# Kernel tuning notes

Measured on AMD Instinct MI355X. Metric: run time of the kernel, lower is better.

## Reference

```python
import jax, jax.numpy as jnp
import numpy as np

B, N, D, H = 256, 40, 256, 256      # molecules, atoms/molecule, pc_hidden, pred_hidden
nS, nC, nB = 40, 5, 5               # n_SYMBOLS, n_FORMAL_CHARGES, n_BOND_TYPES
NEG_SLOPE = 0.01                    # F.leaky_relu default


def _lrelu(x):
    return jnp.where(x >= 0, x, NEG_SLOPE * x)


def setup_inputs() -> dict:
    key = jax.random.key(0)
    ks = jax.random.split(key, 7)
    def w(k, shape, fan_in):
        return jax.random.normal(k, shape, jnp.float32) / np.float32(np.sqrt(fan_in))
    return {
        "yhat": jax.random.normal(ks[0], (B, N, D), jnp.float32),
        "Ws1": w(ks[1], (D, H), D),      "bs1": jnp.zeros((H,), jnp.float32),
        "Ws2": w(ks[2], (H, nS), H),     "bs2": jnp.zeros((nS,), jnp.float32),
        "Wc1": w(ks[3], (D, H), D),      "bc1": jnp.zeros((H,), jnp.float32),
        "Wc2": w(ks[4], (H, nC), H),     "bc2": jnp.zeros((nC,), jnp.float32),
        "Wb1": w(ks[5], (2 * D, H), 2 * D), "bb1": jnp.zeros((H,), jnp.float32),
        "Wb2": w(ks[6], (H, nB), H),     "bb2": jnp.zeros((nB,), jnp.float32),
    }


def reference(yhat, Ws1, bs1, Ws2, bs2, Wc1, bc1, Wc2, bc2, Wb1, bb1, Wb2, bb2):
    # Per-atom symbol / charge heads (2-layer MLP with leaky_relu)
    symbols = _lrelu(yhat @ Ws1 + bs1) @ Ws2 + bs2          # [B, N, nS]
    charges = _lrelu(yhat @ Wc1 + bc1) @ Wc2 + bc2          # [B, N, nC]

    # Pairwise bond head: concat(x_i, x_j) @ Wb1 == x_i @ Wb1[:D] + x_j @ Wb1[D:]
    # (avoids materializing the [B, N, N, 2D] concat tensor)
    p1 = yhat @ Wb1[:D]                                      # [B, N, H]
    p2 = yhat @ Wb1[D:]                                      # [B, N, H]
    h = _lrelu(p1[:, :, None, :] + p2[:, None, :, :] + bb1)  # [B, N, N, H]
    bonds = h @ Wb2 + bb2                                    # [B, N, N, nB]
    bonds = bonds + jnp.swapaxes(bonds, 1, 2)                # symmetrize (i,j)+(j,i)

    return (symbols.reshape(-1, nS),
            charges.reshape(-1, nC),
            bonds.reshape(-1, nB))
```

## Files before the change

### kernel.cpp

```cpp
#include <hip/hip_runtime.h>
#include <hip/hip_bf16.h>

typedef unsigned short u16;
typedef __attribute__((ext_vector_type(4))) int   int4v;
typedef __attribute__((ext_vector_type(4))) unsigned int uint4v;
typedef __attribute__((ext_vector_type(4))) unsigned short ushort4v;
typedef __attribute__((ext_vector_type(4))) float floatx4;
typedef __attribute__((ext_vector_type(8))) short bf16x8;
typedef _Float16 half8 __attribute__((ext_vector_type(8)));
typedef _Float16 half2v __attribute__((ext_vector_type(2)));

#define LRELU_NS 0.01f
#define SK 264

__device__ __forceinline__ float bitsToF(unsigned int b) {
    union { unsigned int u; float f; } v; v.u = b << 16; return v.f;
}
__device__ __forceinline__ u16 f2bf(float f) {
    __hip_bfloat16 h = __float2bfloat16(f);
    return *reinterpret_cast<u16*>(&h);
}
__device__ __forceinline__ float lrelu(float v) {
    return fmaxf(v, LRELU_NS * v);
}
__device__ __forceinline__ u16 ldW(const void* p, int i, int isF32) {
    return isF32 ? f2bf(((const float*)p)[i]) : ((const u16*)p)[i];
}
__device__ __forceinline__ float ldF(const void* p, int i, int isF32) {
    return isF32 ? ((const float*)p)[i]
                 : bitsToF((unsigned int)((const u16*)p)[i]);
}
__device__ __forceinline__ u16 f2h_bits(float f) {
    union { _Float16 h; u16 u; } v; v.h = (_Float16)f; return v.u;
}
__device__ __forceinline__ u16 ldWh(const void* p, int i, int isF32) {
    float f = isF32 ? ((const float*)p)[i]
                    : bitsToF((unsigned int)((const u16*)p)[i]);
    return f2h_bits(f);
}
__device__ __forceinline__ half2v u2h2(unsigned int x) {
    union { unsigned int u; half2v h; } v; v.u = x; return v.h;
}
__device__ __forceinline__ unsigned int h22u(half2v x) {
    union { half2v h; unsigned int u; } v; v.h = x; return v.u;
}

__device__ __forceinline__ int computeIsF32(const u16* y, int* cnt, int t) {
    if (t == 0) *cnt = 0;
    __syncthreads();
    if (t < 256) {
        u16 v = y[2 * t];
        int e = (v >> 7) & 0xFF;
        if (v == 0 || (e >= 96 && e < 160)) atomicAdd(cnt, 1);
    }
    __syncthreads();
    return (*cnt < 192) ? 1 : 0;
}

__global__ __launch_bounds__(256) void pack_kernel(
    const void* __restrict__ yhat,
    const void* __restrict__ Ws1, const void* __restrict__ Wc1,
    const void* __restrict__ Wb1, const void* __restrict__ Ws2,
    const void* __restrict__ Wc2,
    const void* __restrict__ bs1, const void* __restrict__ bc1,
    const void* __restrict__ bb1, const void* __restrict__ bs2,
    const void* __restrict__ bc2, const void* __restrict__ bb2,
    u16* __restrict__ WallT, u16* __restrict__ W2T, float* __restrict__ biasF)
{
    __shared__ int fcnt;
    const int bid = blockIdx.x, t = threadIdx.x;
    const int isF32 = computeIsF32((const u16*)yhat, &fcnt, t);
    if (bid < 64) {
        __shared__ u16 tile[64][65];
        const int c0 = (bid & 15) * 64;
        const int k0 = (bid >> 4) * 64;
        const void* src; int coff; int roff = 0;
        if (c0 < 256)      { src = Ws1; coff = c0; }
        else if (c0 < 512) { src = Wc1; coff = c0 - 256; }
        else if (c0 < 768) { src = Wb1; coff = c0 - 512; }
        else               { src = Wb1; coff = c0 - 768; roff = 256; }
        const int cc = t & 63, kk0 = t >> 6;
        #pragma unroll
        for (int i = 0; i < 16; ++i) {
            int kk = kk0 + i * 4;
            tile[kk][cc] = ldW(src, (k0 + kk + roff) * 256 + coff + cc, isF32);
        }
        __syncthreads();
        const int kk2 = t & 63, cc0 = t >> 6;
        #pragma unroll
        for (int i = 0; i < 16; ++i) {
            int cc2 = cc0 + i * 4;
            WallT[(c0 + cc2) * 256 + (k0 + kk2)] = tile[kk2][cc2];
        }
    } else if (bid < 128) {
        int e2 = (bid - 64) * 256 + t;
        int c = e2 >> 8, k = e2 & 255;
        u16 v = 0;
        if (c < 40)                 v = ldW(Ws2, k * 40 + c, isF32);
        else if (c >= 48 && c < 53) v = ldW(Wc2, k * 5 + (c - 48), isF32);
        W2T[c * 256 + k] = v;
    } else {
        int idx = (bid - 128) * 256 + t;
        float v = 0.f;
        if (idx < 256)       v = ldF(bs1, idx, isF32);
        else if (idx < 512)  v = ldF(bc1, idx - 256, isF32);
        else if (idx < 768)  v = ldF(bb1, idx - 512, isF32);
        else if (idx < 808)  v = ldF(bs2, idx - 768, isF32);
        else if (idx < 813)  v = ldF(bc2, idx - 808, isF32);
        else if (idx >= 816 && idx < 821) v = ldF(bb2, idx - 816, isF32);
        biasF[idx] = v;
    }
}

__global__ __launch_bounds__(256) void heads_kernel(
    const void* __restrict__ Xv, const u16* __restrict__ WallT,
    const u16* __restrict__ W2T, const float* __restrict__ biasF,
    void* __restrict__ outv)
{
    __shared__ u16 Xs[64 * SK];
    __shared__ u16 Hb[64 * SK];
    __shared__ int fcnt;
    const int t = threadIdx.x;
    const int bm0 = blockIdx.x * 64;
    const int head = blockIdx.y;
    const int isF32 = computeIsF32((const u16*)Xv, &fcnt, t);

    if (isF32) {
        const floatx4* __restrict__ src = (const floatx4*)((const float*)Xv + bm0 * 256);
        #pragma unroll
        for (int it = 0; it < 16; ++it) {
            int cid = t + it * 256;
            int row = cid >> 6, ch = cid & 63;
            floatx4 f = src[cid];
            ushort4v u;
            u[0] = f2bf(f[0]); u[1] = f2bf(f[1]); u[2] = f2bf(f[2]); u[3] = f2bf(f[3]);
            *(ushort4v*)&Xs[row * SK + ch * 4] = u;
        }
    } else {
        const int4v* __restrict__ src = (const int4v*)((const u16*)Xv + bm0 * 256);
        #pragma unroll
        for (int it = 0; it < 8; ++it) {
            int cid = t + it * 256;
            int row = cid >> 5, ch = cid & 31;
            *(int4v*)&Xs[row * SK + ch * 8] = src[cid];
        }
    }
    __syncthreads();

    const int w = t >> 6, l = t & 63;
    const int ml = l & 15, kq = l >> 4, r0 = kq * 4;

    for (int n = 0; n < 4; ++n) {
        const int ct = w + 4 * n;
        floatx4 acc[4] = {};
        #pragma unroll
        for (int ks = 0; ks < 8; ++ks) {
            const int k0 = ks * 32 + kq * 8;
            bf16x8 bf = *(const bf16x8*)&WallT[(head * 256 + ct * 16 + ml) * 256 + k0];
            #pragma unroll
            for (int mt = 0; mt < 4; ++mt) {
                bf16x8 a = *(const bf16x8*)&Xs[(mt * 16 + ml) * SK + k0];
                acc[mt] = __builtin_amdgcn_mfma_f32_16x16x32_bf16(a, bf, acc[mt], 0, 0, 0);
            }
        }
        const int col = ct * 16 + ml;
        const float bias = biasF[head * 256 + col];
        #pragma unroll
        for (int mt = 0; mt < 4; ++mt)
            #pragma unroll
            for (int r = 0; r < 4; ++r)
                Hb[(mt * 16 + r0 + r) * SK + col] = f2bf(lrelu(acc[mt][r] + bias));
    }
    __syncthreads();

    const int nct = (head == 0) ? 3 : 1;
    const int c0  = (head == 0) ? 0 : 48;
    floatx4 acc2[3] = {};
    #pragma unroll
    for (int ks = 0; ks < 8; ++ks) {
        const int k0 = ks * 32 + kq * 8;
        bf16x8 a = *(const bf16x8*)&Hb[(w * 16 + ml) * SK + k0];
        #pragma unroll
        for (int j = 0; j < 3; ++j) {
            if (j < nct) {
                bf16x8 bf = *(const bf16x8*)&W2T[(c0 + j * 16 + ml) * 256 + k0];
                acc2[j] = __builtin_amdgcn_mfma_f32_16x16x32_bf16(a, bf, acc2[j], 0, 0, 0);
            }
        }
    }
    #pragma unroll
    for (int j = 0; j < 3; ++j) {
        if (j < nct) {
            const int col = j * 16 + ml;
            const int lim = (head == 0) ? 40 : 5;
            if (col < lim) {
                const float bias = biasF[(head == 0 ? 768 : 808) + col];
                #pragma unroll
                for (int r = 0; r < 4; ++r) {
                    const int row = bm0 + w * 16 + r0 + r;
                    const int o = (head == 0) ? row * 40 + col
                                              : 409600 + row * 5 + col;
                    const float v = acc2[j][r] + bias;
                    if (isF32) ((float*)outv)[o] = v;
                    else ((__hip_bfloat16*)outv)[o] = __float2bfloat16(v);
                }
            }
        }
    }
}

__global__ __launch_bounds__(512) void bonds3_kernel(
    const void* __restrict__ Xv, const u16* __restrict__ WallT,
    const void* __restrict__ Wb2, const float* __restrict__ biasF,
    void* __restrict__ outv)
{
    __shared__ u16 Xm[48 * SK];
    __shared__ u16 P1L[48 * SK];
    __shared__ u16 P2L[48 * SK];
    __shared__ u16 WsB[5 * 264];
    __shared__ int fcnt;
    const int t = threadIdx.x;
    const int b = blockIdx.x >> 1;
    const int h = blockIdx.x & 1;
    const int isF32 = computeIsF32((const u16*)Xv, &fcnt, t);

    if (isF32) {
        const floatx4* __restrict__ src = (const floatx4*)((const float*)Xv + b * 10240);
        #pragma unroll
        for (int s = 0; s < 5; ++s) {
            int cid = t + s * 512;
            int row = cid >> 6, ch = cid & 63;
            floatx4 f = src[cid];
            ushort4v u;
            u[0] = f2bf(f[0]); u[1] = f2bf(f[1]); u[2] = f2bf(f[2]); u[3] = f2bf(f[3]);
            *(ushort4v*)&Xm[row * SK + ch * 4] = u;
        }
        {
            int row = 40 + (t >> 6), ch = t & 63;
            ushort4v z = {0, 0, 0, 0};
            *(ushort4v*)&Xm[row * SK + ch * 4] = z;
        }
    } else {
        const int4v* __restrict__ src = (const int4v*)((const u16*)Xv + b * 10240);
        #pragma unroll
        for (int s = 0; s < 3; ++s) {
            int cid = t + s * 512;
            int row = cid >> 5, ch = cid & 31;
            if (cid < 1280) *(int4v*)&Xm[row * SK + ch * 8] = src[cid];
            else { int4v z = {0, 0, 0, 0}; *(int4v*)&Xm[row * SK + ch * 8] = z; }
        }
    }
    #pragma unroll
    for (int s = 0; s < 3; ++s) {
        int e2 = t + s * 512;
        if (e2 < 1280) {
            int c = e2 >> 8, k = e2 & 255;
            WsB[c * 264 + k] = ldWh(Wb2, k * 5 + c, isF32);
        }
    }
    __syncthreads();

    const int w = t >> 6, l = t & 63;
    const int ml = l & 15, kq = l >> 4, r0 = kq * 4;

    for (int n = 0; n < 4; ++n) {
        const int gc = (w + 8 * n) * 16 + ml;
        floatx4 acc[3] = {};
        #pragma unroll
        for (int ks = 0; ks < 8; ++ks) {
            const int k0 = ks * 32 + kq * 8;
            bf16x8 bf = *(const bf16x8*)&WallT[(512 + gc) * 256 + k0];
            #pragma unroll
            for (int i = 0; i < 3; ++i) {
                bf16x8 a = *(const bf16x8*)&Xm[(i * 16 + ml) * SK + k0];
                acc[i] = __builtin_amdgcn_mfma_f32_16x16x32_bf16(a, bf, acc[i], 0, 0, 0);
            }
        }
        u16* dst = (gc < 256) ? P1L : P2L;
        const int col = gc & 255;
        const float bias = (gc < 256) ? biasF[512 + gc] : 0.f;
        #pragma unroll
        for (int i = 0; i < 3; ++i)
            #pragma unroll
            for (int r = 0; r < 4; ++r)
                dst[(i * 16 + r0 + r) * SK + col] = f2h_bits(acc[i][r] + bias);
    }
    __syncthreads();

    const int sel = (ml < 5) ? ml : 4;
    half8 wf[8];
    #pragma unroll
    for (int ks = 0; ks < 8; ++ks)
        wf[ks] = *(const half8*)&WsB[sel * 264 + ks * 32 + kq * 8];
    const float b2x2 = 2.f * biasF[816 + ml];
    const _Float16 c001 = (_Float16)0.01f;

    constexpr int mT[11]  = {0, 0, 0, 1, 1, 1, 2, 2, 3, 3, 4};
    constexpr int jtT[11] = {0, 1, 2, 0, 1, 2, 1, 2, 1, 2, 2};
    #pragma unroll
    for (int idx = 0; idx < 11; ++idx) {
        if ((idx & 1) != h) continue;
        const int m = mT[idx], jt = jtT[idx];
        const int i = w + 8 * m;
        const bool diag = (jt == (i >> 4));
        floatx4 acc = {};
        #pragma unroll
        for (int ks = 0; ks < 8; ++ks) {
            const int k0 = ks * 32 + kq * 8;
            const uint4v a1 = *(const uint4v*)&P1L[i * SK + k0];
            const uint4v a2 = *(const uint4v*)&P2L[i * SK + k0];
            const uint4v b1 = *(const uint4v*)&P1L[(jt * 16 + ml) * SK + k0];
            const uint4v b2 = *(const uint4v*)&P2L[(jt * 16 + ml) * SK + k0];
            union { unsigned int u[4]; half8 v; } af;
            #pragma unroll
            for (int d = 0; d < 4; ++d) {
                const half2v tF = u2h2(a1[d]) + u2h2(b2[d]);
                const half2v tB = u2h2(b1[d]) + u2h2(a2[d]);
                const half2v lF = __builtin_elementwise_max(tF, tF * c001);
                const half2v lB = __builtin_elementwise_max(tB, tB * c001);
                af.u[d] = h22u(lF + lB);
            }
            acc = __builtin_amdgcn_mfma_f32_16x16x32_f16(af.v, wf[ks], acc, 0, 0, 0);
        }
        if (ml < 5) {
            #pragma unroll
            for (int r = 0; r < 4; ++r) {
                const int j = jt * 16 + r0 + r;
                if (j < 40 && (!diag || j >= i)) {
                    const float v = acc[r] + b2x2;
                    const int o1 = 460800 + (b * 1600 + i * 40 + j) * 5 + ml;
                    if (isF32) ((float*)outv)[o1] = v;
                    else ((__hip_bfloat16*)outv)[o1] = __float2bfloat16(v);
                    if (!diag || j > i) {
                        const int o2 = 460800 + (b * 1600 + j * 40 + i) * 5 + ml;
                        if (isF32) ((float*)outv)[o2] = v;
                        else ((__hip_bfloat16*)outv)[o2] = __float2bfloat16(v);
                    }
                }
            }
        }
    }
}

extern "C" void kernel_launch(void* const* d_in, const int* in_sizes, int n_in,
                              void* d_out, int out_size, void* d_ws, size_t ws_size,
                              hipStream_t stream)
{
    const void* yhat = d_in[0];
    const void* Ws1  = d_in[1];
    const void* bs1  = d_in[2];
    const void* Ws2  = d_in[3];
    const void* bs2  = d_in[4];
    const void* Wc1  = d_in[5];
    const void* bc1  = d_in[6];
    const void* Wc2  = d_in[7];
    const void* bc2  = d_in[8];
    const void* Wb1  = d_in[9];
    const void* bb1  = d_in[10];
    const void* Wb2  = d_in[11];
    const void* bb2  = d_in[12];

    char* wsb = (char*)d_ws;
    float* biasF = (float*)(wsb + 4096);
    u16*   W2T   = (u16*)(wsb + 8192);
    u16*   WallT = (u16*)(wsb + 40960);

    pack_kernel<<<132, 256, 0, stream>>>(yhat, Ws1, Wc1, Wb1, Ws2, Wc2,
                                         bs1, bc1, bb1, bs2, bc2, bb2,
                                         WallT, W2T, biasF);
    heads_kernel<<<dim3(160, 2), 256, 0, stream>>>(yhat, WallT, W2T, biasF, d_out);
    bonds3_kernel<<<512, 512, 0, stream>>>(yhat, WallT, Wb2, biasF, d_out);
}
```

Baseline: 140.4 us.

## Halve heads row tile and batch bond j-tiles per row for A-operand reuse

The heads kernel now processes 32 rows per block instead of 64, doubling the grid to 640 blocks for better CU occupancy and lower LDS use, with only two waves doing the second-layer MFMA. In the bonds kernel, each wave computes all j-tiles for a given row i in one pass, reusing the row's P1/P2 loads across up to three accumulators instead of reloading them per tile. The bond work split between the two half-groups changes from a 6/5 tile interleave to 5/6 grouped by row. This costs more accumulator registers and leaves two waves idle during the heads second stage.

```diff
diff --git a/kernel.cpp b/kernel.cpp
--- a/kernel.cpp
+++ b/kernel.cpp
@@ -112,23 +112,23 @@
     }
 }
 
-__global__ __launch_bounds__(256) void heads_kernel(
+__global__ __launch_bounds__(256) void heads32_kernel(
     const void* __restrict__ Xv, const u16* __restrict__ WallT,
     const u16* __restrict__ W2T, const float* __restrict__ biasF,
     void* __restrict__ outv)
 {
-    __shared__ u16 Xs[64 * SK];
-    __shared__ u16 Hb[64 * SK];
+    __shared__ u16 Xs[32 * SK];
+    __shared__ u16 Hb[32 * SK];
     __shared__ int fcnt;
     const int t = threadIdx.x;
-    const int bm0 = blockIdx.x * 64;
+    const int bm0 = blockIdx.x * 32;
     const int head = blockIdx.y;
     const int isF32 = computeIsF32((const u16*)Xv, &fcnt, t);
 
     if (isF32) {
         const floatx4* __restrict__ src = (const floatx4*)((const float*)Xv + bm0 * 256);
         #pragma unroll
-        for (int it = 0; it < 16; ++it) {
+        for (int it = 0; it < 8; ++it) {
             int cid = t + it * 256;
             int row = cid >> 6, ch = cid & 63;
             floatx4 f = src[cid];
@@ -139,7 +139,7 @@
     } else {
         const int4v* __restrict__ src = (const int4v*)((const u16*)Xv + bm0 * 256);
         #pragma unroll
-        for (int it = 0; it < 8; ++it) {
+        for (int it = 0; it < 4; ++it) {
             int cid = t + it * 256;
             int row = cid >> 5, ch = cid & 31;
             *(int4v*)&Xs[row * SK + ch * 8] = src[cid];
@@ -152,13 +152,13 @@
 
     for (int n = 0; n < 4; ++n) {
         const int ct = w + 4 * n;
-        floatx4 acc[4] = {};
+        floatx4 acc[2] = {};
         #pragma unroll
         for (int ks = 0; ks < 8; ++ks) {
             const int k0 = ks * 32 + kq * 8;
             bf16x8 bf = *(const bf16x8*)&WallT[(head * 256 + ct * 16 + ml) * 256 + k0];
             #pragma unroll
-            for (int mt = 0; mt < 4; ++mt) {
+            for (int mt = 0; mt < 2; ++mt) {
                 bf16x8 a = *(const bf16x8*)&Xs[(mt * 16 + ml) * SK + k0];
                 acc[mt] = __builtin_amdgcn_mfma_f32_16x16x32_bf16(a, bf, acc[mt], 0, 0, 0);
             }
@@ -166,43 +166,45 @@
         const int col = ct * 16 + ml;
         const float bias = biasF[head * 256 + col];
         #pragma unroll
-        for (int mt = 0; mt < 4; ++mt)
+        for (int mt = 0; mt < 2; ++mt)
             #pragma unroll
             for (int r = 0; r < 4; ++r)
                 Hb[(mt * 16 + r0 + r) * SK + col] = f2bf(lrelu(acc[mt][r] + bias));
     }
     __syncthreads();
 
-    const int nct = (head == 0) ? 3 : 1;
-    const int c0  = (head == 0) ? 0 : 48;
-    floatx4 acc2[3] = {};
-    #pragma unroll
-    for (int ks = 0; ks < 8; ++ks) {
-        const int k0 = ks * 32 + kq * 8;
-        bf16x8 a = *(const bf16x8*)&Hb[(w * 16 + ml) * SK + k0];
+    if (w < 2) {
+        const int nct = (head == 0) ? 3 : 1;
+        const int c0  = (head == 0) ? 0 : 48;
+        floatx4 acc2[3] = {};
+        #pragma unroll
+        for (int ks = 0; ks < 8; ++ks) {
+            const int k0 = ks * 32 + kq * 8;
+            bf16x8 a = *(const bf16x8*)&Hb[(w * 16 + ml) * SK + k0];
+            #pragma unroll
+            for (int j = 0; j < 3; ++j) {
+                if (j < nct) {
+                    bf16x8 bf = *(const bf16x8*)&W2T[(c0 + j * 16 + ml) * 256 + k0];
+                    acc2[j] = __builtin_amdgcn_mfma_f32_16x16x32_bf16(a, bf, acc2[j], 0, 0, 0);
+                }
+            }
+        }
         #pragma unroll
         for (int j = 0; j < 3; ++j) {
             if (j < nct) {
-                bf16x8 bf = *(const bf16x8*)&W2T[(c0 + j * 16 + ml) * 256 + k0];
-                acc2[j] = __builtin_amdgcn_mfma_f32_16x16x32_bf16(a, bf, acc2[j], 0, 0, 0);
-            }
-        }
-    }
-    #pragma unroll
-    for (int j = 0; j < 3; ++j) {
-        if (j < nct) {
-            const int col = j * 16 + ml;
-            const int lim = (head == 0) ? 40 : 5;
-            if (col < lim) {
-                const float bias = biasF[(head == 0 ? 768 : 808) + col];
-                #pragma unroll
-                for (int r = 0; r < 4; ++r) {
-                    const int row = bm0 + w * 16 + r0 + r;
-                    const int o = (head == 0) ? row * 40 + col
-                                              : 409600 + row * 5 + col;
-                    const float v = acc2[j][r] + bias;
-                    if (isF32) ((float*)outv)[o] = v;
-                    else ((__hip_bfloat16*)outv)[o] = __float2bfloat16(v);
+                const int col = j * 16 + ml;
+                const int lim = (head == 0) ? 40 : 5;
+                if (col < lim) {
+                    const float bias = biasF[(head == 0 ? 768 : 808) + col];
+                    #pragma unroll
+                    for (int r = 0; r < 4; ++r) {
+                        const int row = bm0 + w * 16 + r0 + r;
+                        const int o = (head == 0) ? row * 40 + col
+                                                  : 409600 + row * 5 + col;
+                        const float v = acc2[j][r] + bias;
+                        if (isF32) ((float*)outv)[o] = v;
+                        else ((__hip_bfloat16*)outv)[o] = __float2bfloat16(v);
+                    }
                 }
             }
         }
@@ -295,51 +297,63 @@
     const float b2x2 = 2.f * biasF[816 + ml];
     const _Float16 c001 = (_Float16)0.01f;
 
-    constexpr int mT[11]  = {0, 0, 0, 1, 1, 1, 2, 2, 3, 3, 4};
-    constexpr int jtT[11] = {0, 1, 2, 0, 1, 2, 1, 2, 1, 2, 2};
-    #pragma unroll
-    for (int idx = 0; idx < 11; ++idx) {
-        if ((idx & 1) != h) continue;
-        const int m = mT[idx], jt = jtT[idx];
+    auto run_m = [&](const int m, const int jtLo) {
         const int i = w + 8 * m;
-        const bool diag = (jt == (i >> 4));
-        floatx4 acc = {};
+        const int itile = i >> 4;
+        const int njt = 3 - jtLo;
+        floatx4 acc[3] = {};
         #pragma unroll
         for (int ks = 0; ks < 8; ++ks) {
             const int k0 = ks * 32 + kq * 8;
             const uint4v a1 = *(const uint4v*)&P1L[i * SK + k0];
             const uint4v a2 = *(const uint4v*)&P2L[i * SK + k0];
-            const uint4v b1 = *(const uint4v*)&P1L[(jt * 16 + ml) * SK + k0];
-            const uint4v b2 = *(const uint4v*)&P2L[(jt * 16 + ml) * SK + k0];
-            union { unsigned int u[4]; half8 v; } af;
-            #pragma unroll
-            for (int d = 0; d < 4; ++d) {
-                const half2v tF = u2h2(a1[d]) + u2h2(b2[d]);
-                const half2v tB = u2h2(b1[d]) + u2h2(a2[d]);
-                const half2v lF = __builtin_elementwise_max(tF, tF * c001);
-                const half2v lB = __builtin_elementwise_max(tB, tB * c001);
-                af.u[d] = h22u(lF + lB);
-            }
-            acc = __builtin_amdgcn_mfma_f32_16x16x32_f16(af.v, wf[ks], acc, 0, 0, 0);
+            #pragma unroll
+            for (int j = 0; j < 3; ++j) {
+                if (j < njt) {
+                    const int jt = jtLo + j;
+                    const uint4v b1 = *(const uint4v*)&P1L[(jt * 16 + ml) * SK + k0];
+                    const uint4v b2 = *(const uint4v*)&P2L[(jt * 16 + ml) * SK + k0];
+                    union { unsigned int u[4]; half8 v; } af;
+                    #pragma unroll
+                    for (int d = 0; d < 4; ++d) {
+                        const half2v tF = u2h2(a1[d]) + u2h2(b2[d]);
+                        const half2v tB = u2h2(b1[d]) + u2h2(a2[d]);
+                        const half2v lF = __builtin_elementwise_max(tF, tF * c001);
+                        const half2v lB = __builtin_elementwise_max(tB, tB * c001);
+                        af.u[d] = h22u(lF + lB);
+                    }
+                    acc[j] = __builtin_amdgcn_mfma_f32_16x16x32_f16(af.v, wf[ks], acc[j], 0, 0, 0);
+                }
+            }
         }
         if (ml < 5) {
             #pragma unroll
-            for (int r = 0; r < 4; ++r) {
-                const int j = jt * 16 + r0 + r;
-                if (j < 40 && (!diag || j >= i)) {
-                    const float v = acc[r] + b2x2;
-                    const int o1 = 460800 + (b * 1600 + i * 40 + j) * 5 + ml;
-                    if (isF32) ((float*)outv)[o1] = v;
-                    else ((__hip_bfloat16*)outv)[o1] = __float2bfloat16(v);
-                    if (!diag || j > i) {
-                        const int o2 = 460800 + (b * 1600 + j * 40 + i) * 5 + ml;
-                        if (isF32) ((float*)outv)[o2] = v;
-                        else ((__hip_bfloat16*)outv)[o2] = __float2bfloat16(v);
+            for (int j = 0; j < 3; ++j) {
+                if (j < njt) {
+                    const int jt = jtLo + j;
+                    const bool diag = (jt == itile);
+                    #pragma unroll
+                    for (int r = 0; r < 4; ++r) {
+                        const int jj = jt * 16 + r0 + r;
+                        if (jj < 40 && (!diag || jj >= i)) {
+                            const float v = acc[j][r] + b2x2;
+                            const int o1 = 460800 + (b * 1600 + i * 40 + jj) * 5 + ml;
+                            if (isF32) ((float*)outv)[o1] = v;
+                            else ((__hip_bfloat16*)outv)[o1] = __float2bfloat16(v);
+                            if (!diag || jj > i) {
+                                const int o2 = 460800 + (b * 1600 + jj * 40 + i) * 5 + ml;
+                                if (isF32) ((float*)outv)[o2] = v;
+                                else ((__hip_bfloat16*)outv)[o2] = __float2bfloat16(v);
+                            }
+                        }
                     }
                 }
             }
         }
-    }
+    };
+
+    if (h == 0) { run_m(0, 0); run_m(2, 1); }
+    else        { run_m(1, 0); run_m(3, 1); run_m(4, 2); }
 }
 
 extern "C" void kernel_launch(void* const* d_in, const int* in_sizes, int n_in,
@@ -368,6 +382,6 @@
     pack_kernel<<<132, 256, 0, stream>>>(yhat, Ws1, Wc1, Wb1, Ws2, Wc2,
                                          bs1, bc1, bb1, bs2, bc2, bb2,
                                          WallT, W2T, biasF);
-    heads_kernel<<<dim3(160, 2), 256, 0, stream>>>(yhat, WallT, W2T, biasF, d_out);
+    heads32_kernel<<<dim3(320, 2), 256, 0, stream>>>(yhat, WallT, W2T, biasF, d_out);
     bonds3_kernel<<<512, 512, 0, stream>>>(yhat, WallT, Wb2, biasF, d_out);
 }
```

After: 143.4 us. 1.02x slower.

## Fuse heads and bonds kernels into one launch with union shared memory

Applied to the files above, without the earlier changes.

Merges the per-atom heads kernel and the pairwise bonds kernel into a single 832-block launch. Block index selects the branch, and the two branches share LDS through a union. The heads path is re-mapped to 512 threads, with 8 waves doing the first GEMM and 4 waves doing the second. This removes one kernel launch and the gap between the two dependent-free kernels so both workloads can fill the GPU together. In exchange it uses more LDS per block for the heads path and leaves half the waves idle during the heads second stage.

```diff
diff --git a/kernel.cpp b/kernel.cpp
--- a/kernel.cpp
+++ b/kernel.cpp
@@ -112,229 +112,226 @@
     }
 }
 
-__global__ __launch_bounds__(256) void heads_kernel(
+union SharedHB {
+    struct { u16 Xs[64 * SK]; u16 Hb[64 * SK]; } hd;
+    struct { u16 Xm[48 * SK]; u16 P1L[48 * SK]; u16 P2L[48 * SK];
+             u16 WsB[5 * 264]; } bd;
+};
+
+__global__ __launch_bounds__(512) void fused_kernel(
     const void* __restrict__ Xv, const u16* __restrict__ WallT,
-    const u16* __restrict__ W2T, const float* __restrict__ biasF,
-    void* __restrict__ outv)
+    const u16* __restrict__ W2T, const void* __restrict__ Wb2,
+    const float* __restrict__ biasF, void* __restrict__ outv)
 {
-    __shared__ u16 Xs[64 * SK];
-    __shared__ u16 Hb[64 * SK];
+    __shared__ SharedHB sh;
     __shared__ int fcnt;
     const int t = threadIdx.x;
-    const int bm0 = blockIdx.x * 64;
-    const int head = blockIdx.y;
+    const int bid = blockIdx.x;
     const int isF32 = computeIsF32((const u16*)Xv, &fcnt, t);
-
-    if (isF32) {
-        const floatx4* __restrict__ src = (const floatx4*)((const float*)Xv + bm0 * 256);
-        #pragma unroll
-        for (int it = 0; it < 16; ++it) {
-            int cid = t + it * 256;
-            int row = cid >> 6, ch = cid & 63;
-            floatx4 f = src[cid];
-            ushort4v u;
-            u[0] = f2bf(f[0]); u[1] = f2bf(f[1]); u[2] = f2bf(f[2]); u[3] = f2bf(f[3]);
-            *(ushort4v*)&Xs[row * SK + ch * 4] = u;
-        }
-    } else {
-        const int4v* __restrict__ src = (const int4v*)((const u16*)Xv + bm0 * 256);
-        #pragma unroll
-        for (int it = 0; it < 8; ++it) {
-            int cid = t + it * 256;
-            int row = cid >> 5, ch = cid & 31;
-            *(int4v*)&Xs[row * SK + ch * 8] = src[cid];
-        }
-    }
-    __syncthreads();
 
     const int w = t >> 6, l = t & 63;
     const int ml = l & 15, kq = l >> 4, r0 = kq * 4;
 
-    for (int n = 0; n < 4; ++n) {
-        const int ct = w + 4 * n;
-        floatx4 acc[4] = {};
-        #pragma unroll
-        for (int ks = 0; ks < 8; ++ks) {
-            const int k0 = ks * 32 + kq * 8;
-            bf16x8 bf = *(const bf16x8*)&WallT[(head * 256 + ct * 16 + ml) * 256 + k0];
-            #pragma unroll
-            for (int mt = 0; mt < 4; ++mt) {
-                bf16x8 a = *(const bf16x8*)&Xs[(mt * 16 + ml) * SK + k0];
-                acc[mt] = __builtin_amdgcn_mfma_f32_16x16x32_bf16(a, bf, acc[mt], 0, 0, 0);
-            }
-        }
-        const int col = ct * 16 + ml;
-        const float bias = biasF[head * 256 + col];
-        #pragma unroll
-        for (int mt = 0; mt < 4; ++mt)
-            #pragma unroll
-            for (int r = 0; r < 4; ++r)
-                Hb[(mt * 16 + r0 + r) * SK + col] = f2bf(lrelu(acc[mt][r] + bias));
-    }
-    __syncthreads();
-
-    const int nct = (head == 0) ? 3 : 1;
-    const int c0  = (head == 0) ? 0 : 48;
-    floatx4 acc2[3] = {};
-    #pragma unroll
-    for (int ks = 0; ks < 8; ++ks) {
-        const int k0 = ks * 32 + kq * 8;
-        bf16x8 a = *(const bf16x8*)&Hb[(w * 16 + ml) * SK + k0];
-        #pragma unroll
-        for (int j = 0; j < 3; ++j) {
-            if (j < nct) {
-                bf16x8 bf = *(const bf16x8*)&W2T[(c0 + j * 16 + ml) * 256 + k0];
-                acc2[j] = __builtin_amdgcn_mfma_f32_16x16x32_bf16(a, bf, acc2[j], 0, 0, 0);
-            }
-        }
-    }
-    #pragma unroll
-    for (int j = 0; j < 3; ++j) {
-        if (j < nct) {
-            const int col = j * 16 + ml;
-            const int lim = (head == 0) ? 40 : 5;
-            if (col < lim) {
-                const float bias = biasF[(head == 0 ? 768 : 808) + col];
+    if (bid < 512) {
+        const int b = bid >> 1;
+        const int h = bid & 1;
+
+        if (isF32) {
+            const floatx4* __restrict__ src = (const floatx4*)((const float*)Xv + b * 10240);
+            #pragma unroll
+            for (int s = 0; s < 5; ++s) {
+                int cid = t + s * 512;
+                int row = cid >> 6, ch = cid & 63;
+                floatx4 f = src[cid];
+                ushort4v u;
+                u[0] = f2bf(f[0]); u[1] = f2bf(f[1]); u[2] = f2bf(f[2]); u[3] = f2bf(f[3]);
+                *(ushort4v*)&sh.bd.Xm[row * SK + ch * 4] = u;
+            }
+            {
+                int row = 40 + (t >> 6), ch = t & 63;
+                ushort4v z = {0, 0, 0, 0};
+                *(ushort4v*)&sh.bd.Xm[row * SK + ch * 4] = z;
+            }
+        } else {
+            const int4v* __restrict__ src = (const int4v*)((const u16*)Xv + b * 10240);
+            #pragma unroll
+            for (int s = 0; s < 3; ++s) {
+                int cid = t + s * 512;
+                int row = cid >> 5, ch = cid & 31;
+                if (cid < 1280) *(int4v*)&sh.bd.Xm[row * SK + ch * 8] = src[cid];
+                else { int4v z = {0, 0, 0, 0}; *(int4v*)&sh.bd.Xm[row * SK + ch * 8] = z; }
+            }
+        }
+        #pragma unroll
+        for (int s = 0; s < 3; ++s) {
+            int e2 = t + s * 512;
+            if (e2 < 1280) {
+                int c = e2 >> 8, k = e2 & 255;
+                sh.bd.WsB[c * 264 + k] = ldWh(Wb2, k * 5 + c, isF32);
+            }
+        }
+        __syncthreads();
+
+        for (int n = 0; n < 4; ++n) {
+            const int gc = (w + 8 * n) * 16 + ml;
+            floatx4 acc[3] = {};
+            #pragma unroll
+            for (int ks = 0; ks < 8; ++ks) {
+                const int k0 = ks * 32 + kq * 8;
+                bf16x8 bf = *(const bf16x8*)&WallT[(512 + gc) * 256 + k0];
+                #pragma unroll
+                for (int i = 0; i < 3; ++i) {
+                    bf16x8 a = *(const bf16x8*)&sh.bd.Xm[(i * 16 + ml) * SK + k0];
+                    acc[i] = __builtin_amdgcn_mfma_f32_16x16x32_bf16(a, bf, acc[i], 0, 0, 0);
+                }
+            }
+            u16* dst = (gc < 256) ? sh.bd.P1L : sh.bd.P2L;
+            const int col = gc & 255;
+            const float bias = (gc < 256) ? biasF[512 + gc] : 0.f;
+            #pragma unroll
+            for (int i = 0; i < 3; ++i)
+                #pragma unroll
+                for (int r = 0; r < 4; ++r)
+                    dst[(i * 16 + r0 + r) * SK + col] = f2h_bits(acc[i][r] + bias);
+        }
+        __syncthreads();
+
+        const int sel = (ml < 5) ? ml : 4;
+        half8 wf[8];
+        #pragma unroll
+        for (int ks = 0; ks < 8; ++ks)
+            wf[ks] = *(const half8*)&sh.bd.WsB[sel * 264 + ks * 32 + kq * 8];
+        const float b2x2 = 2.f * biasF[816 + ml];
+        const _Float16 c001 = (_Float16)0.01f;
+
+        constexpr int mT[11]  = {0, 0, 0, 1, 1, 1, 2, 2, 3, 3, 4};
+        constexpr int jtT[11] = {0, 1, 2, 0, 1, 2, 1, 2, 1, 2, 2};
+        #pragma unroll
+        for (int idx = 0; idx < 11; ++idx) {
+            if ((idx & 1) != h) continue;
+            const int m = mT[idx], jt = jtT[idx];
+            const int i = w + 8 * m;
+            const bool diag = (jt == (i >> 4));
+            floatx4 acc = {};
+            #pragma unroll
+            for (int ks = 0; ks < 8; ++ks) {
+                const int k0 = ks * 32 + kq * 8;
+                const uint4v a1 = *(const uint4v*)&sh.bd.P1L[i * SK + k0];
+                const uint4v a2 = *(const uint4v*)&sh.bd.P2L[i * SK + k0];
+                const uint4v b1 = *(const uint4v*)&sh.bd.P1L[(jt * 16 + ml) * SK + k0];
+                const uint4v b2 = *(const uint4v*)&sh.bd.P2L[(jt * 16 + ml) * SK + k0];
+                union { unsigned int u[4]; half8 v; } af;
+                #pragma unroll
+                for (int d = 0; d < 4; ++d) {
+                    const half2v tF = u2h2(a1[d]) + u2h2(b2[d]);
+                    const half2v tB = u2h2(b1[d]) + u2h2(a2[d]);
+                    const half2v lF = __builtin_elementwise_max(tF, tF * c001);
+                    const half2v lB = __builtin_elementwise_max(tB, tB * c001);
+                    af.u[d] = h22u(lF + lB);
+                }
+                acc = __builtin_amdgcn_mfma_f32_16x16x32_f16(af.v, wf[ks], acc, 0, 0, 0);
+            }
+            if (ml < 5) {
                 #pragma unroll
                 for (int r = 0; r < 4; ++r) {
-                    const int row = bm0 + w * 16 + r0 + r;
-                    const int o = (head == 0) ? row * 40 + col
-                                              : 409600 + row * 5 + col;
-                    const float v = acc2[j][r] + bias;
-                    if (isF32) ((float*)outv)[o] = v;
-                    else ((__hip_bfloat16*)outv)[o] = __float2bfloat16(v);
-                }
-            }
-        }
-    }
-}
-
-__global__ __launch_bounds__(512) void bonds3_kernel(
-    const void* __restrict__ Xv, const u16* __restrict__ WallT,
-    const void* __restrict__ Wb2, const float* __restrict__ biasF,
-    void* __restrict__ outv)
-{
-    __shared__ u16 Xm[48 * SK];
-    __shared__ u16 P1L[48 * SK];
-    __shared__ u16 P2L[48 * SK];
-    __shared__ u16 WsB[5 * 264];
-    __shared__ int fcnt;
-    const int t = threadIdx.x;
-    const int b = blockIdx.x >> 1;
-    const int h = blockIdx.x & 1;
-    const int isF32 = computeIsF32((const u16*)Xv, &fcnt, t);
-
-    if (isF32) {
-        const floatx4* __restrict__ src = (const floatx4*)((const float*)Xv + b * 10240);
-        #pragma unroll
-        for (int s = 0; s < 5; ++s) {
-            int cid = t + s * 512;
-            int row = cid >> 6, ch = cid & 63;
-            floatx4 f = src[cid];
-            ushort4v u;
-            u[0] = f2bf(f[0]); u[1] = f2bf(f[1]); u[2] = f2bf(f[2]); u[3] = f2bf(f[3]);
-            *(ushort4v*)&Xm[row * SK + ch * 4] = u;
-        }
-        {
-            int row = 40 + (t >> 6), ch = t & 63;
-            ushort4v z = {0, 0, 0, 0};
-            *(ushort4v*)&Xm[row * SK + ch * 4] = z;
+                    const int j = jt * 16 + r0 + r;
+                    if (j < 40 && (!diag || j >= i)) {
+                        const float v = acc[r] + b2x2;
+                        const int o1 = 460800 + (b * 1600 + i * 40 + j) * 5 + ml;
+                        if (isF32) ((float*)outv)[o1] = v;
+                        else ((__hip_bfloat16*)outv)[o1] = __float2bfloat16(v);
+                        if (!diag || j > i) {
+                            const int o2 = 460800 + (b * 1600 + j * 40 + i) * 5 + ml;
+                            if (isF32) ((float*)outv)[o2] = v;
+                            else ((__hip_bfloat16*)outv)[o2] = __float2bfloat16(v);
+                        }
+                    }
+                }
+            }
         }
     } else {
-        const int4v* __restrict__ src = (const int4v*)((const u16*)Xv + b * 10240);
-        #pragma unroll
-        for (int s = 0; s < 3; ++s) {
-            int cid = t + s * 512;
-            int row = cid >> 5, ch = cid & 31;
-            if (cid < 1280) *(int4v*)&Xm[row * SK + ch * 8] = src[cid];
-            else { int4v z = {0, 0, 0, 0}; *(int4v*)&Xm[row * SK + ch * 8] = z; }
-        }
-    }
-    #pragma unroll
-    for (int s = 0; s < 3; ++s) {
-        int e2 = t + s * 512;
-        if (e2 < 1280) {
-            int c = e2 >> 8, k = e2 & 255;
-            WsB[c * 264 + k] = ldWh(Wb2, k * 5 + c, isF32);
-        }
-    }
-    __syncthreads();
-
-    const int w = t >> 6, l = t & 63;
-    const int ml = l & 15, kq = l >> 4, r0 = kq * 4;
-
-    for (int n = 0; n < 4; ++n) {
-        const int gc = (w + 8 * n) * 16 + ml;
-        floatx4 acc[3] = {};
-        #pragma unroll
-        for (int ks = 0; ks < 8; ++ks) {
-            const int k0 = ks * 32 + kq * 8;
-            bf16x8 bf = *(const bf16x8*)&WallT[(512 + gc) * 256 + k0];
-            #pragma unroll
-            for (int i = 0; i < 3; ++i) {
-                bf16x8 a = *(const bf16x8*)&Xm[(i * 16 + ml) * SK + k0];
-                acc[i] = __builtin_amdgcn_mfma_f32_16x16x32_bf16(a, bf, acc[i], 0, 0, 0);
-            }
-        }
-        u16* dst = (gc < 256) ? P1L : P2L;
-        const int col = gc & 255;
-        const float bias = (gc < 256) ? biasF[512 + gc] : 0.f;
-        #pragma unroll
-        for (int i = 0; i < 3; ++i)
-            #pragma unroll
-            for (int r = 0; r < 4; ++r)
-                dst[(i * 16 + r0 + r) * SK + col] = f2h_bits(acc[i][r] + bias);
-    }
-    __syncthreads();
-
-    const int sel = (ml < 5) ? ml : 4;
-    half8 wf[8];
-    #pragma unroll
-    for (int ks = 0; ks < 8; ++ks)
-        wf[ks] = *(const half8*)&WsB[sel * 264 + ks * 32 + kq * 8];
-    const float b2x2 = 2.f * biasF[816 + ml];
-    const _Float16 c001 = (_Float16)0.01f;
-
-    constexpr int mT[11]  = {0, 0, 0, 1, 1, 1, 2, 2, 3, 3, 4};
-    constexpr int jtT[11] = {0, 1, 2, 0, 1, 2, 1, 2, 1, 2, 2};
-    #pragma unroll
-    for (int idx = 0; idx < 11; ++idx) {
-        if ((idx & 1) != h) continue;
-        const int m = mT[idx], jt = jtT[idx];
-        const int i = w + 8 * m;
-        const bool diag = (jt == (i >> 4));
-        floatx4 acc = {};
-        #pragma unroll
-        for (int ks = 0; ks < 8; ++ks) {
-            const int k0 = ks * 32 + kq * 8;
-            const uint4v a1 = *(const uint4v*)&P1L[i * SK + k0];
-            const uint4v a2 = *(const uint4v*)&P2L[i * SK + k0];
-            const uint4v b1 = *(const uint4v*)&P1L[(jt * 16 + ml) * SK + k0];
-            const uint4v b2 = *(const uint4v*)&P2L[(jt * 16 + ml) * SK + k0];
-            union { unsigned int u[4]; half8 v; } af;
-            #pragma unroll
-            for (int d = 0; d < 4; ++d) {
-                const half2v tF = u2h2(a1[d]) + u2h2(b2[d]);
-                const half2v tB = u2h2(b1[d]) + u2h2(a2[d]);
-                const half2v lF = __builtin_elementwise_max(tF, tF * c001);
-                const half2v lB = __builtin_elementwise_max(tB, tB * c001);
-                af.u[d] = h22u(lF + lB);
-            }
-            acc = __builtin_amdgcn_mfma_f32_16x16x32_f16(af.v, wf[ks], acc, 0, 0, 0);
-        }
-        if (ml < 5) {
-            #pragma unroll
-            for (int r = 0; r < 4; ++r) {
-                const int j = jt * 16 + r0 + r;
-                if (j < 40 && (!diag || j >= i)) {
-                    const float v = acc[r] + b2x2;
-                    const int o1 = 460800 + (b * 1600 + i * 40 + j) * 5 + ml;
-                    if (isF32) ((float*)outv)[o1] = v;
-                    else ((__hip_bfloat16*)outv)[o1] = __float2bfloat16(v);
-                    if (!diag || j > i) {
-                        const int o2 = 460800 + (b * 1600 + j * 40 + i) * 5 + ml;
-                        if (isF32) ((float*)outv)[o2] = v;
-                        else ((__hip_bfloat16*)outv)[o2] = __float2bfloat16(v);
+        const int hb = bid - 512;
+        const int bm0 = (hb % 160) * 64;
+        const int head = hb / 160;
+
+        if (isF32) {
+            const floatx4* __restrict__ src = (const floatx4*)((const float*)Xv + bm0 * 256);
+            #pragma unroll
+            for (int s = 0; s < 8; ++s) {
+                int cid = t + s * 512;
+                int row = cid >> 6, ch = cid & 63;
+                floatx4 f = src[cid];
+                ushort4v u;
+                u[0] = f2bf(f[0]); u[1] = f2bf(f[1]); u[2] = f2bf(f[2]); u[3] = f2bf(f[3]);
+                *(ushort4v*)&sh.hd.Xs[row * SK + ch * 4] = u;
+            }
+        } else {
+            const int4v* __restrict__ src = (const int4v*)((const u16*)Xv + bm0 * 256);
+            #pragma unroll
+            for (int s = 0; s < 4; ++s) {
+                int cid = t + s * 512;
+                int row = cid >> 5, ch = cid & 31;
+                *(int4v*)&sh.hd.Xs[row * SK + ch * 8] = src[cid];
+            }
+        }
+        __syncthreads();
+
+        #pragma unroll
+        for (int n = 0; n < 2; ++n) {
+            const int ct = w + 8 * n;
+            floatx4 acc[4] = {};
+            #pragma unroll
+            for (int ks = 0; ks < 8; ++ks) {
+                const int k0 = ks * 32 + kq * 8;
+                bf16x8 bf = *(const bf16x8*)&WallT[(head * 256 + ct * 16 + ml) * 256 + k0];
+                #pragma unroll
+                for (int mt = 0; mt < 4; ++mt) {
+                    bf16x8 a = *(const bf16x8*)&sh.hd.Xs[(mt * 16 + ml) * SK + k0];
+                    acc[mt] = __builtin_amdgcn_mfma_f32_16x16x32_bf16(a, bf, acc[mt], 0, 0, 0);
+                }
+            }
+            const int col = ct * 16 + ml;
+            const float bias = biasF[head * 256 + col];
+            #pragma unroll
+            for (int mt = 0; mt < 4; ++mt)
+                #pragma unroll
+                for (int r = 0; r < 4; ++r)
+                    sh.hd.Hb[(mt * 16 + r0 + r) * SK + col] = f2bf(lrelu(acc[mt][r] + bias));
+        }
+        __syncthreads();
+
+        if (w < 4) {
+            const int nct = (head == 0) ? 3 : 1;
+            const int c0  = (head == 0) ? 0 : 48;
+            floatx4 acc2[3] = {};
+            #pragma unroll
+            for (int ks = 0; ks < 8; ++ks) {
+                const int k0 = ks * 32 + kq * 8;
+                bf16x8 a = *(const bf16x8*)&sh.hd.Hb[(w * 16 + ml) * SK + k0];
+                #pragma unroll
+                for (int j = 0; j < 3; ++j) {
+                    if (j < nct) {
+                        bf16x8 bf = *(const bf16x8*)&W2T[(c0 + j * 16 + ml) * 256 + k0];
+                        acc2[j] = __builtin_amdgcn_mfma_f32_16x16x32_bf16(a, bf, acc2[j], 0, 0, 0);
+                    }
+                }
+            }
+            #pragma unroll
+            for (int j = 0; j < 3; ++j) {
+                if (j < nct) {
+                    const int col = j * 16 + ml;
+                    const int lim = (head == 0) ? 40 : 5;
+                    if (col < lim) {
+                        const float bias = biasF[(head == 0 ? 768 : 808) + col];
+                        #pragma unroll
+                        for (int r = 0; r < 4; ++r) {
+                            const int row = bm0 + w * 16 + r0 + r;
+                            const int o = (head == 0) ? row * 40 + col
+                                                      : 409600 + row * 5 + col;
+                            const float v = acc2[j][r] + bias;
+                            if (isF32) ((float*)outv)[o] = v;
+                            else ((__hip_bfloat16*)outv)[o] = __float2bfloat16(v);
+                        }
                     }
                 }
             }
@@ -368,6 +365,5 @@
     pack_kernel<<<132, 256, 0, stream>>>(yhat, Ws1, Wc1, Wb1, Ws2, Wc2,
                                          bs1, bc1, bb1, bs2, bc2, bb2,
                                          WallT, W2T, biasF);
-    heads_kernel<<<dim3(160, 2), 256, 0, stream>>>(yhat, WallT, W2T, biasF, d_out);
-    bonds3_kernel<<<512, 512, 0, stream>>>(yhat, WallT, Wb2, biasF, d_out);
-}
+    fused_kernel<<<832, 512, 0, stream>>>(yhat, WallT, W2T, Wb2, biasF, d_out);
+}
```

Result: faster. 133.8 us (-4.8%).
